# Performance work log

Hardware: AMD Instinct MI355X
Metric: run time of the kernel (lower is better)

The kernel has to match this reference:

```python
import jax, jax.numpy as jnp
import numpy as np

B, T, A, H, E = 256, 64, 32, 512, 32


def setup_inputs() -> dict:
    key = jax.random.key(0)
    ks = jax.random.split(key, 8)
    return {
        "actions": jax.random.normal(ks[0], (B, T, A), dtype=jnp.float32),
        "timesteps": jax.random.randint(ks[1], (B,), 0, 1000, dtype=jnp.int32),
        "cat_ids": jax.random.randint(ks[2], (B,), 0, E, dtype=jnp.int32),
        "W1": 0.02 * jax.random.normal(ks[3], (E, A, H), dtype=jnp.float32),
        "b1": jnp.zeros((E, H), dtype=jnp.float32),
        "W2": 0.02 * jax.random.normal(ks[4], (E, 2 * H, H), dtype=jnp.float32),
        "b2": jnp.zeros((E, H), dtype=jnp.float32),
        "W3": 0.02 * jax.random.normal(ks[5], (E, H, H), dtype=jnp.float32),
        "b3": jnp.zeros((E, H), dtype=jnp.float32),
    }


def _cat_linear(x, cat_ids, W, b):
    # per-sample weight gather + bmm, faithful to torch W[cat_ids]; bmm
    return jnp.einsum("btd,bdh->bth", x, W[cat_ids]) + b[cat_ids][:, None, :]


def _sinusoidal(timesteps_bt, dim):
    half = dim // 2
    exponent = -jnp.arange(half, dtype=jnp.float32) * (jnp.log(jnp.float32(10000.0)) / half)
    freqs = timesteps_bt[..., None] * jnp.exp(exponent)  # (B,T,half)
    return jnp.concatenate([jnp.sin(freqs), jnp.cos(freqs)], axis=-1)


def _swish(x):
    return x * jax.nn.sigmoid(x)


def reference(actions, timesteps, cat_ids, W1, b1, W2, b2, W3, b3):
    Bb, Tt, _ = actions.shape
    t_bt = jnp.broadcast_to(timesteps.astype(jnp.float32)[:, None], (Bb, Tt))
    a_emb = _cat_linear(actions, cat_ids, W1, b1)                     # (B,T,H)
    tau_emb = _sinusoidal(t_bt, a_emb.shape[-1]).astype(a_emb.dtype)  # (B,T,H)
    x = jnp.concatenate([a_emb, tau_emb], axis=-1)                    # (B,T,2H)
    x = _swish(_cat_linear(x, cat_ids, W2, b2))
    return _cat_linear(x, cat_ids, W3, b3)
```

## Files before the change

### kernel.cpp

```cpp
#include <hip/hip_runtime.h>
#include <hip/hip_bf16.h>

#define NB 256
#define NT 64
#define NA 32
#define NH 512
#define NE 32
#define MAXTILES 144

typedef short short8 __attribute__((ext_vector_type(8)));
typedef unsigned short ushort8v __attribute__((ext_vector_type(8)));
typedef float f32x4 __attribute__((ext_vector_type(4)));

__device__ __forceinline__ unsigned short f2bf(float f) {
  unsigned int u = __float_as_uint(f);
  u += 0x7FFFu + ((u >> 16) & 1u);
  return (unsigned short)(u >> 16);
}

__device__ __forceinline__ void gl2lds16(const void* g, void* l) {
  __builtin_amdgcn_global_load_lds(
      (const __attribute__((address_space(1))) unsigned int*)g,
      (__attribute__((address_space(3))) unsigned int*)l, 16, 0, 0);
}

__device__ __forceinline__ ushort8v cvt8(float4 a, float4 b) {
  ushort8v t;
  t[0] = f2bf(a.x); t[1] = f2bf(a.y); t[2] = f2bf(a.z); t[3] = f2bf(a.w);
  t[4] = f2bf(b.x); t[5] = f2bf(b.y); t[6] = f2bf(b.z); t[7] = f2bf(b.w);
  return t;
}

__global__ __launch_bounds__(256) void groupk(const int* __restrict__ cat,
                                              int* __restrict__ tiles,
                                              int* __restrict__ ntiles_out,
                                              int* __restrict__ orderG,
                                              int* __restrict__ offG,
                                              int* __restrict__ cntG) {
  __shared__ int cnt[NE], off[NE], cur[NE];
  __shared__ int order[NB];
  int tid = threadIdx.x;
  if (tid < NE) cnt[tid] = 0;
  __syncthreads();
  int e = cat[tid];
  atomicAdd(&cnt[e], 1);
  __syncthreads();
  if (tid == 0) {
    int s = 0;
    for (int i = 0; i < NE; i++) { off[i] = s; cur[i] = s; s += cnt[i]; }
  }
  __syncthreads();
  int p = atomicAdd(&cur[e], 1);
  order[p] = tid;
  __syncthreads();
  orderG[tid] = order[tid];
  if (tid < NE) { offG[tid] = off[tid]; cntG[tid] = cnt[tid]; }
  if (tid == 0) {
    int nt = 0;
    for (int i = 0; i < NE; i++) {
      for (int j = 0; j < cnt[i]; j += 2) {
        tiles[3 * nt + 0] = i;
        tiles[3 * nt + 1] = order[off[i] + j];
        tiles[3 * nt + 2] = (j + 1 < cnt[i]) ? order[off[i] + j + 1] : -1;
        nt++;
      }
    }
    *ntiles_out = nt;
  }
}

__device__ __forceinline__ void pf_w2(float2 (&pf)[8], const float* __restrict__ W2en,
                                      int k0, int tid) {
#pragma unroll
  for (int j = 0; j < 8; j++) {
    int u = j * 256 + tid;
    int kk = u >> 5, cc = u & 31;
    pf[j] = *(const float2*)(W2en + ((size_t)(k0 + kk) << 9) + cc * 2);
  }
}

__device__ __forceinline__ void pf_w1(float4 (&pfw)[2], const float* __restrict__ W1e,
                                      int k0, int tid) {
  int a = tid >> 3, p = tid & 7;
  const float* src = W1e + (size_t)a * NH + k0 + p * 8;
  pfw[0] = *(const float4*)src;
  pfw[1] = *(const float4*)(src + 4);
}

__device__ __forceinline__ void tau_stage(unsigned short* tauS,
                                          const int* __restrict__ timesteps,
                                          const int* __restrict__ orderG,
                                          int off, int c, int sg, int tid) {
  const float kLog = 0.035977893400931146f;
  for (int j = 0; j < 32; j++) {
    int u = j * 256 + tid;
    int s = u >> 9, k = u & 511;
    int si = sg * 16 + s;
    float t = (si < c) ? (float)timesteps[orderG[off + si]] : 0.f;
    float f = expf(-(float)(k & 255) * kLog);
    float ang = t * f;
    tauS[s * 520 + k] = f2bf((k < 256) ? sinf(ang) : cosf(ang));
  }
}

__global__ __launch_bounds__(256) void wp_kernel(
    const float* __restrict__ W1, const float* __restrict__ b1,
    const float* __restrict__ W2, const float* __restrict__ b2,
    const int* __restrict__ timesteps, const int* __restrict__ orderG,
    const int* __restrict__ offG, const int* __restrict__ cntG,
    unsigned short* __restrict__ Wt12, float* __restrict__ tvec,
    const float* __restrict__ W3, unsigned short* __restrict__ Wt3) {
  __shared__ __align__(16) unsigned char smem[50176];
  int tid = threadIdx.x;

  if (blockIdx.x >= 256) {
    float* S = (float*)smem;
    int id = blockIdx.x - 256;
    int e = id >> 6, rem = id & 63;
    int nt = (rem & 7) * 64, kt = (rem >> 3) * 64;
#pragma unroll
    for (int j = 0; j < 8; j++) {
      int u = j * 256 + tid;
      int k = u >> 5, c = u & 31;
      float2 v = *(const float2*)(W3 + ((size_t)e * 512 + kt + k) * NH + nt + 2 * c);
      *(float2*)(&S[k * 66 + 2 * c]) = v;
    }
    __syncthreads();
#pragma unroll
    for (int j = 0; j < 2; j++) {
      int u = j * 256 + tid;
      int n = u >> 3, c = u & 7;
      ushort8v pk;
#pragma unroll
      for (int jj = 0; jj < 8; jj++) pk[jj] = f2bf(S[(c * 8 + jj) * 66 + n]);
      *(ushort8v*)(Wt3 + ((size_t)e * NH + nt + n) * 512 + kt + c * 8) = pk;
    }
    return;
  }

  float* S            = (float*)smem;
  unsigned short* Bs  = (unsigned short*)(smem + 16896);
  unsigned short* As  = (unsigned short*)(smem + 25088);
  unsigned short* tauS= (unsigned short*)(smem + 29184);
  float* b1S          = (float*)(smem + 45824);
  float* bias2P       = (float*)(smem + 47872);
  float* bias2S       = (float*)(smem + 49920);

  int bxx = blockIdx.x;
  int e = bxx >> 3, n0 = (bxx & 7) * 64;
  int w = tid >> 6, l = tid & 63;
  int lrow = l & 15, kq = l >> 4;
  int tn = tid & 63, tp = tid >> 6;
  int c = cntG[e], off = offG[e];

  const float* W2en = W2 + ((size_t)e << 19) + n0;
  const float* W1e = W1 + ((size_t)e << 14);

  {
    float2 v = *(const float2*)(b1 + (size_t)e * NH + tid * 2);
    *(float2*)(&b1S[tid * 2]) = v;
  }
  tau_stage(tauS, timesteps, orderG, off, c, 0, tid);

  float2 pf[2][8];
  float4 pfW[2][2];
  pf_w2(pf[0], W2en, 0, tid);
  pf_w1(pfW[0], W1e, 0, tid);

  f32x4 acc1[2];
  acc1[0] = (f32x4){0.f, 0.f, 0.f, 0.f};
  acc1[1] = (f32x4){0.f, 0.f, 0.f, 0.f};
  f32x4 acc2 = (f32x4){0.f, 0.f, 0.f, 0.f};
  float bacc0 = 0.f, bacc1 = 0.f;

#pragma unroll
  for (int chunk = 0; chunk < 16; chunk++) {
    const int cur = chunk & 1, nxt = cur ^ 1;
    __syncthreads();
#pragma unroll
    for (int j = 0; j < 8; j++) {
      int u = j * 256 + tid;
      int kk = u >> 5, cc = u & 31;
      *(float2*)(&S[kk * 66 + cc * 2]) = pf[cur][j];
    }
    if (chunk < 15) pf_w2(pf[nxt], W2en, (chunk + 1) * 64, tid);
    if (chunk < 8) {
      int a = tid >> 3, p = tid & 7;
      *(ushort8v*)(&As[a * 64 + (p ^ (a & 7)) * 8]) = cvt8(pfW[cur][0], pfW[cur][1]);
      if (chunk < 7) pf_w1(pfW[nxt], W1e, (chunk + 1) * 64, tid);
    }
    __syncthreads();
#pragma unroll
    for (int i2 = 0; i2 < 2; i2++) {
      int p = tp + i2 * 4;
      ushort8v pk;
      float bsum = 0.f;
#pragma unroll
      for (int jj = 0; jj < 8; jj++) {
        float sv = S[(p * 8 + jj) * 66 + tn];
        pk[jj] = f2bf(sv);
        if (chunk < 8) bsum += sv * b1S[chunk * 64 + p * 8 + jj];
      }
      *(ushort8v*)(&Bs[tn * 64 + (p ^ (tn & 7)) * 8]) = pk;
      if (chunk < 8) { if (i2 == 0) bacc0 += bsum; else bacc1 += bsum; }
    }
    __syncthreads();
    if (chunk < 8) {
#pragma unroll
      for (int s2 = 0; s2 < 2; s2++) {
        int nrow = w * 16 + lrow;
        short8 bf = *(short8*)(&Bs[nrow * 64 + (((s2 * 4 + kq) ^ (nrow & 7))) * 8]);
#pragma unroll
        for (int mi = 0; mi < 2; mi++) {
          int ar = mi * 16 + lrow;
          short8 af = *(short8*)(&As[ar * 64 + (((s2 * 4 + kq) ^ (ar & 7))) * 8]);
          acc1[mi] = __builtin_amdgcn_mfma_f32_16x16x32_bf16(af, bf, acc1[mi], 0, 0, 0);
        }
      }
    } else {
#pragma unroll
      for (int s2 = 0; s2 < 2; s2++) {
        int nrow = w * 16 + lrow;
        short8 bf = *(short8*)(&Bs[nrow * 64 + (((s2 * 4 + kq) ^ (nrow & 7))) * 8]);
        short8 af = *(short8*)(&tauS[lrow * 520 + (chunk - 8) * 64 + s2 * 32 + kq * 8]);
        acc2 = __builtin_amdgcn_mfma_f32_16x16x32_bf16(af, bf, acc2, 0, 0, 0);
      }
    }
  }

  unsigned short* Sb = (unsigned short*)S;
#pragma unroll
  for (int mi = 0; mi < 2; mi++)
#pragma unroll
    for (int r = 0; r < 4; r++)
      Sb[(w * 16 + lrow) * 40 + mi * 16 + kq * 4 + r] = f2bf(acc1[mi][r]);
  bias2P[tn * 8 + tp] = bacc0;
  bias2P[tn * 8 + tp + 4] = bacc1;
  __syncthreads();
  if (tid < 64) {
    float s = b2[(size_t)e * NH + n0 + tid];
#pragma unroll
    for (int p2 = 0; p2 < 8; p2++) s += bias2P[tid * 8 + p2];
    bias2S[tid] = s;
  }
  {
    int n = tid >> 2, q = tid & 3;
    ushort8v v = *(ushort8v*)(&Sb[n * 40 + q * 8]);
    *(ushort8v*)(Wt12 + ((size_t)(e * NH) + n0 + n) * NA + q * 8) = v;
  }
  __syncthreads();

  {
    float bb = bias2S[w * 16 + lrow];
#pragma unroll
    for (int r = 0; r < 4; r++) {
      int si = kq * 4 + r;
      if (si < c)
        tvec[(size_t)orderG[off + si] * NH + n0 + w * 16 + lrow] = acc2[r] + bb;
    }
  }

  for (int sg = 1; sg * 16 < c; sg++) {
    __syncthreads();
    tau_stage(tauS, timesteps, orderG, off, c, sg, tid);
    pf_w2(pf[0], W2en, 512, tid);
    f32x4 acc2b = (f32x4){0.f, 0.f, 0.f, 0.f};
#pragma unroll
    for (int chunk = 8; chunk < 16; chunk++) {
      const int cur = chunk & 1, nxt = cur ^ 1;
      __syncthreads();
#pragma unroll
      for (int j = 0; j < 8; j++) {
        int u = j * 256 + tid;
        int kk = u >> 5, cc = u & 31;
        *(float2*)(&S[kk * 66 + cc * 2]) = pf[cur][j];
      }
      if (chunk < 15) pf_w2(pf[nxt], W2en, (chunk + 1) * 64, tid);
      __syncthreads();
#pragma unroll
      for (int i2 = 0; i2 < 2; i2++) {
        int p = tp + i2 * 4;
        ushort8v pk;
#pragma unroll
        for (int jj = 0; jj < 8; jj++) pk[jj] = f2bf(S[(p * 8 + jj) * 66 + tn]);
        *(ushort8v*)(&Bs[tn * 64 + (p ^ (tn & 7)) * 8]) = pk;
      }
      __syncthreads();
#pragma unroll
      for (int s2 = 0; s2 < 2; s2++) {
        int nrow = w * 16 + lrow;
        short8 bf = *(short8*)(&Bs[nrow * 64 + (((s2 * 4 + kq) ^ (nrow & 7))) * 8]);
        short8 af = *(short8*)(&tauS[lrow * 520 + (chunk - 8) * 64 + s2 * 32 + kq * 8]);
        acc2b = __builtin_amdgcn_mfma_f32_16x16x32_bf16(af, bf, acc2b, 0, 0, 0);
      }
    }
    float bb = bias2S[w * 16 + lrow];
#pragma unroll
    for (int r = 0; r < 4; r++) {
      int si = sg * 16 + kq * 4 + r;
      if (si < c)
        tvec[(size_t)orderG[off + si] * NH + n0 + w * 16 + lrow] = acc2b[r] + bb;
    }
  }
}

__global__ __launch_bounds__(256) void gemmh_kernel(
    const float* __restrict__ actions, const unsigned short* __restrict__ Wt12,
    const float* __restrict__ tvec, const int* __restrict__ cat_ids,
    unsigned short* __restrict__ Hb) {
  __shared__ __align__(16) unsigned char smem[16384 + 5120 + 33792];
  unsigned short* Ws = (unsigned short*)smem;
  unsigned short* As = (unsigned short*)(smem + 16384);
  unsigned short* Ts = (unsigned short*)(smem + 16384 + 5120);

  int b = blockIdx.y, h = blockIdx.x;
  int tid = threadIdx.x;
  int e = cat_ids[b];

  {
    const unsigned short* wsrc = Wt12 + ((size_t)e * NH + h * 256) * NA;
#pragma unroll
    for (int j = 0; j < 4; j++) {
      int u = j * 256 + tid;
      int n = u >> 2, p = u & 3;
      int ch = p ^ ((n >> 1) & 3);
      gl2lds16(wsrc + (size_t)n * NA + ch * 8,
               Ws + (size_t)(j * 256 + (tid & 448)) * 8);
    }
  }
  {
    int row = tid >> 2, seg = tid & 3;
    const float* src = actions + (size_t)(b * NT + row) * NA + seg * 8;
    float4 v0 = *(const float4*)(src);
    float4 v1 = *(const float4*)(src + 4);
    *(ushort8v*)(&As[row * 40 + seg * 8]) = cvt8(v0, v1);
  }
  __syncthreads();

  int w = tid >> 6, l = tid & 63;
  int lrow = l & 15, kq = l >> 4;
  short8 af = *(short8*)(&As[(w * 16 + lrow) * 40 + kq * 8]);
  f32x4 zero = {0.f, 0.f, 0.f, 0.f};
  f32x4 acc[16];
#pragma unroll
  for (int ni = 0; ni < 16; ni++) {
    int nn = ni * 16 + lrow;
    int p = kq ^ ((nn >> 1) & 3);
    short8 bfv = *(short8*)(&Ws[nn * 32 + p * 8]);
    acc[ni] = __builtin_amdgcn_mfma_f32_16x16x32_bf16(af, bfv, zero, 0, 0, 0);
  }
#pragma unroll
  for (int ni = 0; ni < 16; ni++) {
    int colL = ni * 16 + lrow;
    float bv = tvec[(size_t)b * NH + h * 256 + colL];
#pragma unroll
    for (int r = 0; r < 4; r++) {
      int row = w * 16 + kq * 4 + r;
      float v = acc[ni][r] + bv;
      v = v / (1.0f + __expf(-v));
      Ts[row * 264 + colL] = f2bf(v);
    }
  }
  __syncthreads();
#pragma unroll
  for (int i = 0; i < 8; i++) {
    int u = i * 256 + tid;
    int t = u >> 5, c4 = u & 31;
    uint4 v = *(uint4*)(&Ts[t * 264 + c4 * 8]);
    *(uint4*)(Hb + ((size_t)(b * NT + t)) * NH + h * 256 + c4 * 8) = v;
  }
}

template <int KTOT, bool HASTAU, bool SWISH, bool OUT_BF16>
__global__ __launch_bounds__(256) void gemm2_kernel(
    const unsigned short* __restrict__ Xa, const unsigned short* __restrict__ Xt,
    const unsigned short* __restrict__ Wt, const float* __restrict__ bias,
    void* __restrict__ Yv, const int* __restrict__ tiles,
    const int* __restrict__ pntiles) {
  __shared__ __align__(16) unsigned char smem[49152];

  int ti = blockIdx.y;
  if (ti >= *pntiles) return;
  int n0 = blockIdx.x * 64;
  int e = tiles[3 * ti], s0 = tiles[3 * ti + 1], s1 = tiles[3 * ti + 2];
  int s1v = (s1 < 0) ? s0 : s1;

  int tid = threadIdx.x;
  int l = tid & 63;
  int wr = (tid >> 7), wc = (tid >> 6) & 1;
  int lrow = l & 15, kq = l >> 4;

  const unsigned short* wbase = Wt + ((size_t)e * NH + n0) * KTOT;
  constexpr int NIT = KTOT / 64;

  auto stage = [&](int it, int buf) {
    unsigned short* As = (unsigned short*)(smem + buf * 24576);
    unsigned short* Bs = (unsigned short*)(smem + buf * 24576 + 16384);
    int k0 = it * 64;
#pragma unroll
    for (int j = 0; j < 4; j++) {
      int u = j * 256 + tid;
      int row = u >> 3, p = u & 7;
      int ch = p ^ (row & 7);
      int kk = k0 + ch * 8;
      int s = (row < 64) ? s0 : s1v;
      const unsigned short* src;
      if (HASTAU && kk >= 512)
        src = Xt + (size_t)s * NH + (kk - 512);
      else
        src = Xa + ((size_t)(s * NT + (row & 63))) * NH + kk;
      gl2lds16(src, As + (size_t)(j * 256 + (tid & 448)) * 8);
    }
#pragma unroll
    for (int j = 0; j < 2; j++) {
      int u = j * 256 + tid;
      int n = u >> 3, p = u & 7;
      int ch = p ^ (n & 7);
      gl2lds16(wbase + (size_t)n * KTOT + k0 + ch * 8,
               Bs + (size_t)(j * 256 + (tid & 448)) * 8);
    }
  };

  f32x4 acc[4][2];
#pragma unroll
  for (int mi = 0; mi < 4; mi++)
#pragma unroll
    for (int ni = 0; ni < 2; ni++) acc[mi][ni] = (f32x4){0.f, 0.f, 0.f, 0.f};

  stage(0, 0);
  stage(1, 1);

  for (int t = 0; t < NIT; t++) {
    int cur = t & 1;
    unsigned short* As = (unsigned short*)(smem + cur * 24576);
    unsigned short* Bs = (unsigned short*)(smem + cur * 24576 + 16384);

    if (t + 1 < NIT) {
      asm volatile("s_waitcnt vmcnt(6)" ::: "memory");
    } else {
      asm volatile("s_waitcnt vmcnt(0)" ::: "memory");
    }
    __builtin_amdgcn_sched_barrier(0);
    __builtin_amdgcn_s_barrier();
    __builtin_amdgcn_sched_barrier(0);

    short8 afr[2][4], bfr[2][2];
#pragma unroll
    for (int s2 = 0; s2 < 2; s2++) {
#pragma unroll
      for (int mi = 0; mi < 4; mi++) {
        int row = wr * 64 + mi * 16 + lrow;
        int p = (s2 * 4 + kq) ^ (row & 7);
        afr[s2][mi] = *(short8*)(&As[row * 64 + p * 8]);
      }
#pragma unroll
      for (int ni = 0; ni < 2; ni++) {
        int n = wc * 32 + ni * 16 + lrow;
        int p = (s2 * 4 + kq) ^ (n & 7);
        bfr[s2][ni] = *(short8*)(&Bs[n * 64 + p * 8]);
      }
    }
    asm volatile("s_waitcnt lgkmcnt(0)" ::: "memory");
    __builtin_amdgcn_sched_barrier(0);
    __builtin_amdgcn_s_barrier();
    __builtin_amdgcn_sched_barrier(0);

    if (t + 2 < NIT) stage(t + 2, cur);

#pragma unroll
    for (int s2 = 0; s2 < 2; s2++)
#pragma unroll
      for (int mi = 0; mi < 4; mi++)
#pragma unroll
        for (int ni = 0; ni < 2; ni++)
          acc[mi][ni] = __builtin_amdgcn_mfma_f32_16x16x32_bf16(
              afr[s2][mi], bfr[s2][ni], acc[mi][ni], 0, 0, 0);
  }
  __syncthreads();

#pragma unroll
  for (int ni = 0; ni < 2; ni++) {
    int colL = wc * 32 + ni * 16 + lrow;
    float bv = bias[(size_t)e * NH + n0 + colL];
#pragma unroll
    for (int mi = 0; mi < 4; mi++) {
#pragma unroll
      for (int r = 0; r < 4; r++) {
        int row = wr * 64 + mi * 16 + kq * 4 + r;
        float v = acc[mi][ni][r] + bv;
        if (SWISH) v = v / (1.0f + __expf(-v));
        if (OUT_BF16)
          ((unsigned short*)smem)[row * 80 + colL] = f2bf(v);
        else
          ((float*)smem)[row * 68 + colL] = v;
      }
    }
  }
  __syncthreads();
  if (OUT_BF16) {
    unsigned short* Y = (unsigned short*)Yv;
#pragma unroll
    for (int i = 0; i < 4; i++) {
      int u = i * 256 + tid;
      int row = u >> 3, c = u & 7;
      if (row >= 64 && s1 < 0) continue;
      int s = (row < 64) ? s0 : s1;
      uint4 v = *(uint4*)(&((unsigned short*)smem)[row * 80 + c * 8]);
      *(uint4*)(Y + ((size_t)(s * NT + (row & 63))) * NH + n0 + c * 8) = v;
    }
  } else {
    float* Y = (float*)Yv;
#pragma unroll
    for (int i = 0; i < 8; i++) {
      int u = i * 256 + tid;
      int row = u >> 4, c = u & 15;
      if (row >= 64 && s1 < 0) continue;
      int s = (row < 64) ? s0 : s1;
      uint4 v = *(uint4*)(&((float*)smem)[row * 68 + c * 4]);
      *(uint4*)(Y + ((size_t)(s * NT + (row & 63))) * NH + n0 + c * 4) = v;
    }
  }
}

extern "C" void kernel_launch(void* const* d_in, const int* in_sizes, int n_in,
                              void* d_out, int out_size, void* d_ws, size_t ws_size,
                              hipStream_t stream) {
  const float* actions   = (const float*)d_in[0];
  const int*   timesteps = (const int*)d_in[1];
  const int*   cat_ids   = (const int*)d_in[2];
  const float* W1 = (const float*)d_in[3];
  const float* b1 = (const float*)d_in[4];
  const float* W2 = (const float*)d_in[5];
  const float* b2 = (const float*)d_in[6];
  const float* W3 = (const float*)d_in[7];
  const float* b3 = (const float*)d_in[8];

  unsigned short* Hb   = (unsigned short*)d_ws;
  unsigned short* Wt3  = (unsigned short*)((char*)d_ws + (size_t)16777216);
  unsigned short* Wt12 = (unsigned short*)((char*)d_ws + (size_t)33554432);
  float* tvec  = (float*)((char*)d_ws + (size_t)34603008);
  int* tiles   = (int*)((char*)d_ws + (size_t)35192832);
  int* ntiles  = tiles + 3 * MAXTILES;
  int* orderG  = ntiles + 1;
  int* offG    = orderG + NB;
  int* cntG    = offG + NE;

  groupk<<<1, 256, 0, stream>>>(cat_ids, tiles, ntiles, orderG, offG, cntG);
  wp_kernel<<<2304, 256, 0, stream>>>(W1, b1, W2, b2, timesteps, orderG, offG,
                                      cntG, Wt12, tvec, W3, Wt3);
  gemmh_kernel<<<dim3(2, NB), 256, 0, stream>>>(actions, Wt12, tvec, cat_ids, Hb);
  gemm2_kernel<512, false, false, false><<<dim3(8, MAXTILES), 256, 0, stream>>>(
      Hb, nullptr, Wt3, b3, d_out, tiles, ntiles);
}
```

Before: 202.6 us.

## Fold grouping kernel into weight prep and split W2 halves across blocks

Removes the separate single-block grouping launch by running it as an extra block of the weight-prep kernel. Each tau-side block now builds its own per-expert sample list from cat_ids. The W1·W2a fold and the tau·W2b product, which used to run serially in one block over 16 chunks, now run as two independent sets of 256 blocks. The folded bias is written to global memory and added in the hidden GEMM epilogue, so the two halves no longer need to share shared memory. This shortens the critical path per block and drops a launch, at the cost of a duplicated cat scan per tau block and an extra bias read.

```diff
diff --git a/kernel.cpp b/kernel.cpp
--- a/kernel.cpp
+++ b/kernel.cpp
@@ -31,44 +31,6 @@
   return t;
 }
 
-__global__ __launch_bounds__(256) void groupk(const int* __restrict__ cat,
-                                              int* __restrict__ tiles,
-                                              int* __restrict__ ntiles_out,
-                                              int* __restrict__ orderG,
-                                              int* __restrict__ offG,
-                                              int* __restrict__ cntG) {
-  __shared__ int cnt[NE], off[NE], cur[NE];
-  __shared__ int order[NB];
-  int tid = threadIdx.x;
-  if (tid < NE) cnt[tid] = 0;
-  __syncthreads();
-  int e = cat[tid];
-  atomicAdd(&cnt[e], 1);
-  __syncthreads();
-  if (tid == 0) {
-    int s = 0;
-    for (int i = 0; i < NE; i++) { off[i] = s; cur[i] = s; s += cnt[i]; }
-  }
-  __syncthreads();
-  int p = atomicAdd(&cur[e], 1);
-  order[p] = tid;
-  __syncthreads();
-  orderG[tid] = order[tid];
-  if (tid < NE) { offG[tid] = off[tid]; cntG[tid] = cnt[tid]; }
-  if (tid == 0) {
-    int nt = 0;
-    for (int i = 0; i < NE; i++) {
-      for (int j = 0; j < cnt[i]; j += 2) {
-        tiles[3 * nt + 0] = i;
-        tiles[3 * nt + 1] = order[off[i] + j];
-        tiles[3 * nt + 2] = (j + 1 < cnt[i]) ? order[off[i] + j + 1] : -1;
-        nt++;
-      }
-    }
-    *ntiles_out = nt;
-  }
-}
-
 __device__ __forceinline__ void pf_w2(float2 (&pf)[8], const float* __restrict__ W2en,
                                       int k0, int tid) {
 #pragma unroll
@@ -87,35 +49,21 @@
   pfw[1] = *(const float4*)(src + 4);
 }
 
-__device__ __forceinline__ void tau_stage(unsigned short* tauS,
-                                          const int* __restrict__ timesteps,
-                                          const int* __restrict__ orderG,
-                                          int off, int c, int sg, int tid) {
-  const float kLog = 0.035977893400931146f;
-  for (int j = 0; j < 32; j++) {
-    int u = j * 256 + tid;
-    int s = u >> 9, k = u & 511;
-    int si = sg * 16 + s;
-    float t = (si < c) ? (float)timesteps[orderG[off + si]] : 0.f;
-    float f = expf(-(float)(k & 255) * kLog);
-    float ang = t * f;
-    tauS[s * 520 + k] = f2bf((k < 256) ? sinf(ang) : cosf(ang));
-  }
-}
-
 __global__ __launch_bounds__(256) void wp_kernel(
     const float* __restrict__ W1, const float* __restrict__ b1,
     const float* __restrict__ W2, const float* __restrict__ b2,
-    const int* __restrict__ timesteps, const int* __restrict__ orderG,
-    const int* __restrict__ offG, const int* __restrict__ cntG,
-    unsigned short* __restrict__ Wt12, float* __restrict__ tvec,
-    const float* __restrict__ W3, unsigned short* __restrict__ Wt3) {
-  __shared__ __align__(16) unsigned char smem[50176];
+    const float* __restrict__ W3, const int* __restrict__ timesteps,
+    const int* __restrict__ cat, unsigned short* __restrict__ Wt12,
+    float* __restrict__ bias2G, float* __restrict__ tvec,
+    unsigned short* __restrict__ Wt3, int* __restrict__ tiles,
+    int* __restrict__ ntiles_out) {
+  __shared__ __align__(16) unsigned char smem[43008];
   int tid = threadIdx.x;
-
-  if (blockIdx.x >= 256) {
+  int bx = blockIdx.x;
+
+  if (bx >= 512 && bx < 2560) {
     float* S = (float*)smem;
-    int id = blockIdx.x - 256;
+    int id = bx - 512;
     int e = id >> 6, rem = id & 63;
     int nt = (rem & 7) * 64, kt = (rem >> 3) * 64;
 #pragma unroll
@@ -138,74 +86,103 @@
     return;
   }
 
-  float* S            = (float*)smem;
-  unsigned short* Bs  = (unsigned short*)(smem + 16896);
-  unsigned short* As  = (unsigned short*)(smem + 25088);
-  unsigned short* tauS= (unsigned short*)(smem + 29184);
-  float* b1S          = (float*)(smem + 45824);
-  float* bias2P       = (float*)(smem + 47872);
-  float* bias2S       = (float*)(smem + 49920);
-
-  int bxx = blockIdx.x;
-  int e = bxx >> 3, n0 = (bxx & 7) * 64;
+  if (bx == 2560) {
+    int* cnt = (int*)smem;
+    int* off = cnt + 32;
+    int* cur = off + 32;
+    int* order = cur + 32;
+    if (tid < NE) cnt[tid] = 0;
+    __syncthreads();
+    int e = cat[tid];
+    atomicAdd(&cnt[e], 1);
+    __syncthreads();
+    if (tid == 0) {
+      int s = 0;
+      for (int i = 0; i < NE; i++) { off[i] = s; cur[i] = s; s += cnt[i]; }
+    }
+    __syncthreads();
+    int p = atomicAdd(&cur[e], 1);
+    order[p] = tid;
+    __syncthreads();
+    if (tid == 0) {
+      int nt = 0;
+      for (int i = 0; i < NE; i++) {
+        for (int j = 0; j < cnt[i]; j += 2) {
+          tiles[3 * nt + 0] = i;
+          tiles[3 * nt + 1] = order[off[i] + j];
+          tiles[3 * nt + 2] = (j + 1 < cnt[i]) ? order[off[i] + j + 1] : -1;
+          nt++;
+        }
+      }
+      *ntiles_out = nt;
+    }
+    return;
+  }
+
   int w = tid >> 6, l = tid & 63;
   int lrow = l & 15, kq = l >> 4;
   int tn = tid & 63, tp = tid >> 6;
-  int c = cntG[e], off = offG[e];
-
-  const float* W2en = W2 + ((size_t)e << 19) + n0;
-  const float* W1e = W1 + ((size_t)e << 14);
-
-  {
-    float2 v = *(const float2*)(b1 + (size_t)e * NH + tid * 2);
-    *(float2*)(&b1S[tid * 2]) = v;
-  }
-  tau_stage(tauS, timesteps, orderG, off, c, 0, tid);
-
-  float2 pf[2][8];
-  float4 pfW[2][2];
-  pf_w2(pf[0], W2en, 0, tid);
-  pf_w1(pfW[0], W1e, 0, tid);
-
-  f32x4 acc1[2];
-  acc1[0] = (f32x4){0.f, 0.f, 0.f, 0.f};
-  acc1[1] = (f32x4){0.f, 0.f, 0.f, 0.f};
-  f32x4 acc2 = (f32x4){0.f, 0.f, 0.f, 0.f};
-  float bacc0 = 0.f, bacc1 = 0.f;
-
-#pragma unroll
-  for (int chunk = 0; chunk < 16; chunk++) {
-    const int cur = chunk & 1, nxt = cur ^ 1;
-    __syncthreads();
-#pragma unroll
-    for (int j = 0; j < 8; j++) {
-      int u = j * 256 + tid;
-      int kk = u >> 5, cc = u & 31;
-      *(float2*)(&S[kk * 66 + cc * 2]) = pf[cur][j];
-    }
-    if (chunk < 15) pf_w2(pf[nxt], W2en, (chunk + 1) * 64, tid);
-    if (chunk < 8) {
-      int a = tid >> 3, p = tid & 7;
-      *(ushort8v*)(&As[a * 64 + (p ^ (a & 7)) * 8]) = cvt8(pfW[cur][0], pfW[cur][1]);
-      if (chunk < 7) pf_w1(pfW[nxt], W1e, (chunk + 1) * 64, tid);
-    }
-    __syncthreads();
-#pragma unroll
-    for (int i2 = 0; i2 < 2; i2++) {
-      int p = tp + i2 * 4;
-      ushort8v pk;
-      float bsum = 0.f;
-#pragma unroll
-      for (int jj = 0; jj < 8; jj++) {
-        float sv = S[(p * 8 + jj) * 66 + tn];
-        pk[jj] = f2bf(sv);
-        if (chunk < 8) bsum += sv * b1S[chunk * 64 + p * 8 + jj];
-      }
-      *(ushort8v*)(&Bs[tn * 64 + (p ^ (tn & 7)) * 8]) = pk;
-      if (chunk < 8) { if (i2 == 0) bacc0 += bsum; else bacc1 += bsum; }
-    }
-    __syncthreads();
-    if (chunk < 8) {
+
+  if (bx < 256) {
+    float* S            = (float*)smem;
+    unsigned short* Bs  = (unsigned short*)(smem + 16896);
+    unsigned short* As  = (unsigned short*)(smem + 25088);
+    float* b1S          = (float*)(smem + 29184);
+    float* bias2P       = (float*)(smem + 31232);
+
+    int e = bx >> 3, n0 = (bx & 7) * 64;
+    const float* W2en = W2 + ((size_t)e << 19) + n0;
+    const float* W1e = W1 + ((size_t)e << 14);
+
+    {
+      float2 v = *(const float2*)(b1 + (size_t)e * NH + tid * 2);
+      *(float2*)(&b1S[tid * 2]) = v;
+    }
+
+    float2 pf[2][8];
+    float4 pfW[2][2];
+    pf_w2(pf[0], W2en, 0, tid);
+    pf_w1(pfW[0], W1e, 0, tid);
+
+    f32x4 acc1[2];
+    acc1[0] = (f32x4){0.f, 0.f, 0.f, 0.f};
+    acc1[1] = (f32x4){0.f, 0.f, 0.f, 0.f};
+    float bacc0 = 0.f, bacc1 = 0.f;
+
+#pragma unroll
+    for (int chunk = 0; chunk < 8; chunk++) {
+      const int cur = chunk & 1, nxt = cur ^ 1;
+      __syncthreads();
+#pragma unroll
+      for (int j = 0; j < 8; j++) {
+        int u = j * 256 + tid;
+        int kk = u >> 5, cc = u & 31;
+        *(float2*)(&S[kk * 66 + cc * 2]) = pf[cur][j];
+      }
+      {
+        int a = tid >> 3, p = tid & 7;
+        *(ushort8v*)(&As[a * 64 + (p ^ (a & 7)) * 8]) = cvt8(pfW[cur][0], pfW[cur][1]);
+      }
+      if (chunk < 7) {
+        pf_w2(pf[nxt], W2en, (chunk + 1) * 64, tid);
+        pf_w1(pfW[nxt], W1e, (chunk + 1) * 64, tid);
+      }
+      __syncthreads();
+#pragma unroll
+      for (int i2 = 0; i2 < 2; i2++) {
+        int p = tp + i2 * 4;
+        ushort8v pk;
+        float bsum = 0.f;
+#pragma unroll
+        for (int jj = 0; jj < 8; jj++) {
+          float sv = S[(p * 8 + jj) * 66 + tn];
+          pk[jj] = f2bf(sv);
+          bsum += sv * b1S[chunk * 64 + p * 8 + jj];
+        }
+        *(ushort8v*)(&Bs[tn * 64 + (p ^ (tn & 7)) * 8]) = pk;
+        if (i2 == 0) bacc0 += bsum; else bacc1 += bsum;
+      }
+      __syncthreads();
 #pragma unroll
       for (int s2 = 0; s2 < 2; s2++) {
         int nrow = w * 16 + lrow;
@@ -217,97 +194,111 @@
           acc1[mi] = __builtin_amdgcn_mfma_f32_16x16x32_bf16(af, bf, acc1[mi], 0, 0, 0);
         }
       }
-    } else {
-#pragma unroll
-      for (int s2 = 0; s2 < 2; s2++) {
-        int nrow = w * 16 + lrow;
-        short8 bf = *(short8*)(&Bs[nrow * 64 + (((s2 * 4 + kq) ^ (nrow & 7))) * 8]);
-        short8 af = *(short8*)(&tauS[lrow * 520 + (chunk - 8) * 64 + s2 * 32 + kq * 8]);
-        acc2 = __builtin_amdgcn_mfma_f32_16x16x32_bf16(af, bf, acc2, 0, 0, 0);
-      }
-    }
-  }
-
-  unsigned short* Sb = (unsigned short*)S;
-#pragma unroll
-  for (int mi = 0; mi < 2; mi++)
-#pragma unroll
-    for (int r = 0; r < 4; r++)
-      Sb[(w * 16 + lrow) * 40 + mi * 16 + kq * 4 + r] = f2bf(acc1[mi][r]);
-  bias2P[tn * 8 + tp] = bacc0;
-  bias2P[tn * 8 + tp + 4] = bacc1;
-  __syncthreads();
-  if (tid < 64) {
-    float s = b2[(size_t)e * NH + n0 + tid];
-#pragma unroll
-    for (int p2 = 0; p2 < 8; p2++) s += bias2P[tid * 8 + p2];
-    bias2S[tid] = s;
-  }
+    }
+
+    unsigned short* Sb = (unsigned short*)S;
+#pragma unroll
+    for (int mi = 0; mi < 2; mi++)
+#pragma unroll
+      for (int r = 0; r < 4; r++)
+        Sb[(w * 16 + lrow) * 40 + mi * 16 + kq * 4 + r] = f2bf(acc1[mi][r]);
+    bias2P[tn * 8 + tp] = bacc0;
+    bias2P[tn * 8 + tp + 4] = bacc1;
+    __syncthreads();
+    if (tid < 64) {
+      float s = b2[(size_t)e * NH + n0 + tid];
+#pragma unroll
+      for (int p2 = 0; p2 < 8; p2++) s += bias2P[tid * 8 + p2];
+      bias2G[(size_t)e * NH + n0 + tid] = s;
+    }
+    {
+      int n = tid >> 2, q = tid & 3;
+      ushort8v v = *(ushort8v*)(&Sb[n * 40 + q * 8]);
+      *(ushort8v*)(Wt12 + ((size_t)(e * NH) + n0 + n) * NA + q * 8) = v;
+    }
+    return;
+  }
+
   {
-    int n = tid >> 2, q = tid & 3;
-    ushort8v v = *(ushort8v*)(&Sb[n * 40 + q * 8]);
-    *(ushort8v*)(Wt12 + ((size_t)(e * NH) + n0 + n) * NA + q * 8) = v;
-  }
-  __syncthreads();
-
-  {
-    float bb = bias2S[w * 16 + lrow];
-#pragma unroll
-    for (int r = 0; r < 4; r++) {
-      int si = kq * 4 + r;
-      if (si < c)
-        tvec[(size_t)orderG[off + si] * NH + n0 + w * 16 + lrow] = acc2[r] + bb;
-    }
-  }
-
-  for (int sg = 1; sg * 16 < c; sg++) {
-    __syncthreads();
-    tau_stage(tauS, timesteps, orderG, off, c, sg, tid);
-    pf_w2(pf[0], W2en, 512, tid);
-    f32x4 acc2b = (f32x4){0.f, 0.f, 0.f, 0.f};
-#pragma unroll
-    for (int chunk = 8; chunk < 16; chunk++) {
-      const int cur = chunk & 1, nxt = cur ^ 1;
-      __syncthreads();
-#pragma unroll
-      for (int j = 0; j < 8; j++) {
+    float* S            = (float*)smem;
+    unsigned short* Bs  = (unsigned short*)(smem + 16896);
+    unsigned short* tauS= (unsigned short*)(smem + 25088);
+    int* list           = (int*)(smem + 41728);
+    int* pcnt           = (int*)(smem + 42752);
+
+    int id = bx - 256;
+    int e = id >> 3, n0 = (id & 7) * 64;
+    const float* W2bn = W2 + ((size_t)e << 19) + ((size_t)512 << 9) + n0;
+
+    if (tid == 0) *pcnt = 0;
+    __syncthreads();
+    {
+      int ce = cat[tid];
+      if (ce == e) { int p = atomicAdd(pcnt, 1); list[p] = tid; }
+    }
+    __syncthreads();
+    int c = *pcnt;
+    if (c == 0) return;
+
+    const float kLog = 0.035977893400931146f;
+    float2 pf[2][8];
+
+    for (int sg = 0; sg * 16 < c; sg++) {
+      if (sg > 0) __syncthreads();
+      for (int j = 0; j < 32; j++) {
         int u = j * 256 + tid;
-        int kk = u >> 5, cc = u & 31;
-        *(float2*)(&S[kk * 66 + cc * 2]) = pf[cur][j];
-      }
-      if (chunk < 15) pf_w2(pf[nxt], W2en, (chunk + 1) * 64, tid);
-      __syncthreads();
-#pragma unroll
-      for (int i2 = 0; i2 < 2; i2++) {
-        int p = tp + i2 * 4;
-        ushort8v pk;
-#pragma unroll
-        for (int jj = 0; jj < 8; jj++) pk[jj] = f2bf(S[(p * 8 + jj) * 66 + tn]);
-        *(ushort8v*)(&Bs[tn * 64 + (p ^ (tn & 7)) * 8]) = pk;
-      }
-      __syncthreads();
-#pragma unroll
-      for (int s2 = 0; s2 < 2; s2++) {
-        int nrow = w * 16 + lrow;
-        short8 bf = *(short8*)(&Bs[nrow * 64 + (((s2 * 4 + kq) ^ (nrow & 7))) * 8]);
-        short8 af = *(short8*)(&tauS[lrow * 520 + (chunk - 8) * 64 + s2 * 32 + kq * 8]);
-        acc2b = __builtin_amdgcn_mfma_f32_16x16x32_bf16(af, bf, acc2b, 0, 0, 0);
-      }
-    }
-    float bb = bias2S[w * 16 + lrow];
-#pragma unroll
-    for (int r = 0; r < 4; r++) {
-      int si = sg * 16 + kq * 4 + r;
-      if (si < c)
-        tvec[(size_t)orderG[off + si] * NH + n0 + w * 16 + lrow] = acc2b[r] + bb;
+        int s = u >> 9, k = u & 511;
+        int si = sg * 16 + s;
+        float t = (si < c) ? (float)timesteps[list[si]] : 0.f;
+        float f = expf(-(float)(k & 255) * kLog);
+        float ang = t * f;
+        tauS[s * 520 + k] = f2bf((k < 256) ? sinf(ang) : cosf(ang));
+      }
+      pf_w2(pf[0], W2bn, 0, tid);
+      f32x4 acc2 = (f32x4){0.f, 0.f, 0.f, 0.f};
+#pragma unroll
+      for (int chunk = 0; chunk < 8; chunk++) {
+        const int cur = chunk & 1, nxt = cur ^ 1;
+        __syncthreads();
+#pragma unroll
+        for (int j = 0; j < 8; j++) {
+          int u = j * 256 + tid;
+          int kk = u >> 5, cc = u & 31;
+          *(float2*)(&S[kk * 66 + cc * 2]) = pf[cur][j];
+        }
+        if (chunk < 7) pf_w2(pf[nxt], W2bn, (chunk + 1) * 64, tid);
+        __syncthreads();
+#pragma unroll
+        for (int i2 = 0; i2 < 2; i2++) {
+          int p = tp + i2 * 4;
+          ushort8v pk;
+#pragma unroll
+          for (int jj = 0; jj < 8; jj++) pk[jj] = f2bf(S[(p * 8 + jj) * 66 + tn]);
+          *(ushort8v*)(&Bs[tn * 64 + (p ^ (tn & 7)) * 8]) = pk;
+        }
+        __syncthreads();
+#pragma unroll
+        for (int s2 = 0; s2 < 2; s2++) {
+          int nrow = w * 16 + lrow;
+          short8 bf = *(short8*)(&Bs[nrow * 64 + (((s2 * 4 + kq) ^ (nrow & 7))) * 8]);
+          short8 af = *(short8*)(&tauS[lrow * 520 + chunk * 64 + s2 * 32 + kq * 8]);
+          acc2 = __builtin_amdgcn_mfma_f32_16x16x32_bf16(af, bf, acc2, 0, 0, 0);
+        }
+      }
+#pragma unroll
+      for (int r = 0; r < 4; r++) {
+        int si = sg * 16 + kq * 4 + r;
+        if (si < c)
+          tvec[(size_t)list[si] * NH + n0 + w * 16 + lrow] = acc2[r];
+      }
     }
   }
 }
 
 __global__ __launch_bounds__(256) void gemmh_kernel(
     const float* __restrict__ actions, const unsigned short* __restrict__ Wt12,
-    const float* __restrict__ tvec, const int* __restrict__ cat_ids,
-    unsigned short* __restrict__ Hb) {
+    const float* __restrict__ tvec, const float* __restrict__ bias2,
+    const int* __restrict__ cat_ids, unsigned short* __restrict__ Hb) {
   __shared__ __align__(16) unsigned char smem[16384 + 5120 + 33792];
   unsigned short* Ws = (unsigned short*)smem;
   unsigned short* As = (unsigned short*)(smem + 16384);
@@ -352,7 +343,8 @@
 #pragma unroll
   for (int ni = 0; ni < 16; ni++) {
     int colL = ni * 16 + lrow;
-    float bv = tvec[(size_t)b * NH + h * 256 + colL];
+    float bv = tvec[(size_t)b * NH + h * 256 + colL] +
+               bias2[(size_t)e * NH + h * 256 + colL];
 #pragma unroll
     for (int r = 0; r < 4; r++) {
       int row = w * 16 + kq * 4 + r;
@@ -539,16 +531,14 @@
   unsigned short* Wt3  = (unsigned short*)((char*)d_ws + (size_t)16777216);
   unsigned short* Wt12 = (unsigned short*)((char*)d_ws + (size_t)33554432);
   float* tvec  = (float*)((char*)d_ws + (size_t)34603008);
+  float* bias2 = (float*)((char*)d_ws + (size_t)35127296);
   int* tiles   = (int*)((char*)d_ws + (size_t)35192832);
   int* ntiles  = tiles + 3 * MAXTILES;
-  int* orderG  = ntiles + 1;
-  int* offG    = orderG + NB;
-  int* cntG    = offG + NE;
-
-  groupk<<<1, 256, 0, stream>>>(cat_ids, tiles, ntiles, orderG, offG, cntG);
-  wp_kernel<<<2304, 256, 0, stream>>>(W1, b1, W2, b2, timesteps, orderG, offG,
-                                      cntG, Wt12, tvec, W3, Wt3);
-  gemmh_kernel<<<dim3(2, NB), 256, 0, stream>>>(actions, Wt12, tvec, cat_ids, Hb);
+
+  wp_kernel<<<2561, 256, 0, stream>>>(W1, b1, W2, b2, W3, timesteps, cat_ids,
+                                      Wt12, bias2, tvec, Wt3, tiles, ntiles);
+  gemmh_kernel<<<dim3(2, NB), 256, 0, stream>>>(actions, Wt12, tvec, bias2,
+                                                cat_ids, Hb);
   gemm2_kernel<512, false, false, false><<<dim3(8, MAXTILES), 256, 0, stream>>>(
       Hb, nullptr, Wt3, b3, d_out, tiles, ntiles);
 }
```

New measurement: 195.4 us. 1.04x faster.
